# Kernel tuning notes

Hardware: AMD Instinct MI355X
Metric: run time of the kernel (lower is better)

Reference implementation:

```python
import jax, jax.numpy as jnp
import numpy as np

N_NODES = 1_000_000
N_EDGES = 16_000_000
N_GRAPHS = 256
IN_FEATS = 8
DIM = 1
N_LAYERS = 4


def setup_inputs() -> dict:
    key = jax.random.key(0)
    ks = jax.random.split(key, 16)
    x = jax.random.normal(ks[0], (N_NODES, IN_FEATS), dtype=jnp.float32)
    src = jax.random.randint(ks[1], (N_EDGES,), 0, N_NODES, dtype=jnp.int32)
    dst = jax.random.randint(ks[2], (N_EDGES,), 0, N_NODES, dtype=jnp.int32)
    graph_ids = jnp.sort(jax.random.randint(ks[3], (N_NODES,), 0, N_GRAPHS, dtype=jnp.int32))
    s = 1.0 / np.sqrt(IN_FEATS)
    # layer 0: in_feats -> 1 (neighbor GraphConv weight+bias, self linear no bias)
    W0n = jax.random.uniform(ks[4], (IN_FEATS, DIM), jnp.float32, -s, s)
    b0 = jnp.zeros((DIM,), jnp.float32)
    W0s = jax.random.uniform(ks[5], (IN_FEATS, DIM), jnp.float32, -s, s)
    # layers 1..3: 1 -> 1, stacked
    Wkn = jax.random.uniform(ks[6], (N_LAYERS - 1, DIM, DIM), jnp.float32, -1.0, 1.0)
    bk = jnp.zeros((N_LAYERS - 1, DIM), jnp.float32)
    Wks = jax.random.uniform(ks[7], (N_LAYERS - 1, DIM, DIM), jnp.float32, -1.0, 1.0)
    fc1_w = jax.random.uniform(ks[8], (DIM, 8), jnp.float32, -1.0, 1.0)
    fc1_b = jax.random.uniform(ks[9], (8,), jnp.float32, -1.0, 1.0)
    out_w = jax.random.uniform(ks[10], (8, 4), jnp.float32, -1.0 / np.sqrt(8), 1.0 / np.sqrt(8))
    out_b = jax.random.uniform(ks[11], (4,), jnp.float32, -1.0 / np.sqrt(8), 1.0 / np.sqrt(8))
    return {"x": x, "src": src, "dst": dst, "graph_ids": graph_ids, "num_graphs": N_GRAPHS,
            "W0n": W0n, "b0": b0, "W0s": W0s, "Wkn": Wkn, "bk": bk, "Wks": Wks,
            "fc1_w": fc1_w, "fc1_b": fc1_b, "out_w": out_w, "out_b": out_b}


def _graph_conv_wl(x, src, dst, Wn, bn, Ws, n_nodes):
    # GraphConvWL: sum-aggregated neighbor GraphConv (norm='none') + self linear.
    # Apply weight before aggregation (mathematically identical, and cheaper since out_dim=1).
    xw = x @ Wn                                            # [N, out]
    neigh = jax.ops.segment_sum(xw[src], dst, num_segments=n_nodes) + bn
    return neigh + x @ Ws


def reference(x, src, dst, graph_ids, num_graphs, W0n, b0, W0s, Wkn, bk, Wks, fc1_w, fc1_b, out_w, out_b):
    n = x.shape[0]
    h = jax.nn.relu(_graph_conv_wl(x, src, dst, W0n, b0, W0s, n))
    for i in range(Wkn.shape[0]):
        h = jax.nn.relu(_graph_conv_wl(h, src, dst, Wkn[i], bk[i], Wks[i], n))
    hg = jax.ops.segment_sum(h, graph_ids, num_segments=num_graphs)  # [G, 1] readout
    hg2 = jax.nn.sigmoid((hg @ fc1_w + fc1_b) * 1000.0)
    out = jax.nn.relu(hg2 @ out_w + out_b)
    return jax.nn.log_softmax(out, axis=1)
```

## Files before the change

### kernel.cpp

```cpp
#include <hip/hip_runtime.h>
#include <stdint.h>


static constexpr int NGRAPHS    = 256;
static constexpr int TB         = 256;
static constexpr int TB_P       = 512;
static constexpr int PGRID      = 256;
static constexpr int TB_A       = 1024;
static constexpr int BNODE_LOG  = 12;
static constexpr int BNODE      = 1 << BNODE_LOG;
static constexpr int MAXBUCK    = 256;
static constexpr int LOCAL_SHIFT = 20;


__global__ void node_init(const float4* __restrict__ x,
                          const float* __restrict__ W0n,
                          const float* __restrict__ W0s,
                          float* __restrict__ xw0,
                          float* __restrict__ s0,
                          int n_nodes) {
    int n = blockIdx.x * blockDim.x + threadIdx.x;
    if (n >= n_nodes) return;
    float4 a = x[2 * n];
    float4 b = x[2 * n + 1];
    float xn = a.x * W0n[0] + a.y * W0n[1] + a.z * W0n[2] + a.w * W0n[3] +
               b.x * W0n[4] + b.y * W0n[5] + b.z * W0n[6] + b.w * W0n[7];
    float xs = a.x * W0s[0] + a.y * W0s[1] + a.z * W0s[2] + a.w * W0s[3] +
               b.x * W0s[4] + b.y * W0s[5] + b.z * W0s[6] + b.w * W0s[7];
    xw0[n] = xn;
    s0[n] = xs;
}

__global__ void head(const float* __restrict__ hg,
                     const float* __restrict__ fc1_w,
                     const float* __restrict__ fc1_b,
                     const float* __restrict__ out_w,
                     const float* __restrict__ out_b,
                     float* __restrict__ out) {
    int gph = threadIdx.x;
    if (gph >= NGRAPHS) return;
    float hv = hg[gph];
    float o0 = out_b[0], o1 = out_b[1], o2 = out_b[2], o3 = out_b[3];
#pragma unroll
    for (int j = 0; j < 8; ++j) {
        float z = (hv * fc1_w[j] + fc1_b[j]) * 1000.0f;
        float sg = 1.0f / (1.0f + expf(-z));
        o0 += sg * out_w[j * 4 + 0];
        o1 += sg * out_w[j * 4 + 1];
        o2 += sg * out_w[j * 4 + 2];
        o3 += sg * out_w[j * 4 + 3];
    }
    o0 = fmaxf(o0, 0.0f); o1 = fmaxf(o1, 0.0f);
    o2 = fmaxf(o2, 0.0f); o3 = fmaxf(o3, 0.0f);
    float m = fmaxf(fmaxf(o0, o1), fmaxf(o2, o3));
    float s = expf(o0 - m) + expf(o1 - m) + expf(o2 - m) + expf(o3 - m);
    float l = logf(s);
    out[gph * 4 + 0] = o0 - m - l;
    out[gph * 4 + 1] = o1 - m - l;
    out[gph * 4 + 2] = o2 - m - l;
    out[gph * 4 + 3] = o3 - m - l;
}


__global__ void count_bins(const int* __restrict__ dst, int n_edges, int nbuck,
                           int* __restrict__ counts) {
    __shared__ int hist[MAXBUCK];
    for (int i = threadIdx.x; i < MAXBUCK; i += blockDim.x) hist[i] = 0;
    __syncthreads();
    const int4* dst4 = (const int4*)dst;
    int nquads = n_edges >> 2;
    int gtid = blockIdx.x * blockDim.x + threadIdx.x;
    int stride = gridDim.x * blockDim.x;
    for (int q = gtid; q < nquads; q += stride) {
        int4 d = dst4[q];
        atomicAdd(&hist[d.x >> BNODE_LOG], 1);
        atomicAdd(&hist[d.y >> BNODE_LOG], 1);
        atomicAdd(&hist[d.z >> BNODE_LOG], 1);
        atomicAdd(&hist[d.w >> BNODE_LOG], 1);
    }
    if (blockIdx.x == 0) {
        for (int e = (nquads << 2) + threadIdx.x; e < n_edges; e += blockDim.x)
            atomicAdd(&hist[dst[e] >> BNODE_LOG], 1);
    }
    __syncthreads();
    for (int i = threadIdx.x; i < nbuck; i += blockDim.x)
        if (hist[i]) atomicAdd(&counts[i], hist[i]);
}

__global__ void scan_offsets(const int* __restrict__ counts, int nbuck,
                             int* __restrict__ offs, int* __restrict__ cursor) {
    __shared__ int lds[MAXBUCK];
    int i = threadIdx.x;
    int c = (i < nbuck) ? counts[i] : 0;
    lds[i] = c;
    __syncthreads();
    for (int off = 1; off < MAXBUCK; off <<= 1) {
        int v = (i >= off) ? lds[i - off] : 0;
        __syncthreads();
        lds[i] += v;
        __syncthreads();
    }
    int excl = lds[i] - c;
    offs[i] = excl;
    if (i < nbuck) cursor[i] = excl;
    if (i == MAXBUCK - 1) offs[MAXBUCK] = lds[MAXBUCK - 1];
}

__global__ void place_edges(const int* __restrict__ src,
                            const int* __restrict__ dst,
                            int n_edges, int nbuck,
                            int* __restrict__ cursor,
                            uint32_t* __restrict__ sorted) {
    __shared__ int hist[MAXBUCK];
    for (int i = threadIdx.x; i < MAXBUCK; i += blockDim.x) hist[i] = 0;
    __syncthreads();

    const int nquads = n_edges >> 2;
    const int perq = (nquads + gridDim.x - 1) / gridDim.x;
    const int begq = blockIdx.x * perq;
    const int endq = min(begq + perq, nquads);
    const bool last = (blockIdx.x == gridDim.x - 1);
    const int tail_beg = nquads << 2;

    const int4* src4 = (const int4*)src;
    const int4* dst4 = (const int4*)dst;

    for (int q = begq + threadIdx.x; q < endq; q += blockDim.x) {
        int4 d = dst4[q];
        atomicAdd(&hist[d.x >> BNODE_LOG], 1);
        atomicAdd(&hist[d.y >> BNODE_LOG], 1);
        atomicAdd(&hist[d.z >> BNODE_LOG], 1);
        atomicAdd(&hist[d.w >> BNODE_LOG], 1);
    }
    if (last) {
        for (int e = tail_beg + threadIdx.x; e < n_edges; e += blockDim.x)
            atomicAdd(&hist[dst[e] >> BNODE_LOG], 1);
    }
    __syncthreads();
    for (int b = threadIdx.x; b < nbuck; b += blockDim.x) {
        int h = hist[b];
        hist[b] = h ? atomicAdd(&cursor[b], h) : 0;
    }
    __syncthreads();
    for (int q = begq + threadIdx.x; q < endq; q += blockDim.x) {
        int4 d = dst4[q];
        int4 s = src4[q];
        int p0 = atomicAdd(&hist[d.x >> BNODE_LOG], 1);
        int p1 = atomicAdd(&hist[d.y >> BNODE_LOG], 1);
        int p2 = atomicAdd(&hist[d.z >> BNODE_LOG], 1);
        int p3 = atomicAdd(&hist[d.w >> BNODE_LOG], 1);
        sorted[p0] = ((uint32_t)(d.x & (BNODE - 1)) << LOCAL_SHIFT) | (uint32_t)s.x;
        sorted[p1] = ((uint32_t)(d.y & (BNODE - 1)) << LOCAL_SHIFT) | (uint32_t)s.y;
        sorted[p2] = ((uint32_t)(d.z & (BNODE - 1)) << LOCAL_SHIFT) | (uint32_t)s.z;
        sorted[p3] = ((uint32_t)(d.w & (BNODE - 1)) << LOCAL_SHIFT) | (uint32_t)s.w;
    }
    if (last) {
        for (int e = tail_beg + threadIdx.x; e < n_edges; e += blockDim.x) {
            int d = dst[e];
            int pos = atomicAdd(&hist[d >> BNODE_LOG], 1);
            sorted[pos] = ((uint32_t)(d & (BNODE - 1)) << LOCAL_SHIFT) | (uint32_t)src[e];
        }
    }
}


__device__ __forceinline__ void bucket_accumulate(const uint32_t* __restrict__ sorted,
                                                  const int* __restrict__ offs,
                                                  const float* __restrict__ gsrc,
                                                  float* acc) {
    int b = blockIdx.x;
    for (int i = threadIdx.x; i < BNODE; i += TB_A) acc[i] = 0.0f;
    __syncthreads();
    int e = offs[b] + threadIdx.x;
    int eend = offs[b + 1];
    for (; e + 3 * TB_A < eend; e += 4 * TB_A) {
        uint32_t p0 = sorted[e];
        uint32_t p1 = sorted[e + TB_A];
        uint32_t p2 = sorted[e + 2 * TB_A];
        uint32_t p3 = sorted[e + 3 * TB_A];
        float v0 = gsrc[p0 & 0xFFFFFu];
        float v1 = gsrc[p1 & 0xFFFFFu];
        float v2 = gsrc[p2 & 0xFFFFFu];
        float v3 = gsrc[p3 & 0xFFFFFu];
        atomicAdd(&acc[p0 >> LOCAL_SHIFT], v0);
        atomicAdd(&acc[p1 >> LOCAL_SHIFT], v1);
        atomicAdd(&acc[p2 >> LOCAL_SHIFT], v2);
        atomicAdd(&acc[p3 >> LOCAL_SHIFT], v3);
    }
    for (; e < eend; e += TB_A) {
        uint32_t p = sorted[e];
        atomicAdd(&acc[p >> LOCAL_SHIFT], gsrc[p & 0xFFFFFu]);
    }
    __syncthreads();
}

__global__ void layer0_agg(const uint32_t* __restrict__ sorted,
                           const int* __restrict__ offs,
                           const float* __restrict__ xw0,
                           const float* __restrict__ s0,
                           const float* __restrict__ b0,
                           float* __restrict__ h_out,
                           int n_nodes) {
    __shared__ float acc[BNODE];
    bucket_accumulate(sorted, offs, xw0, acc);
    int base = blockIdx.x << BNODE_LOG;
    int nloc = min(BNODE, n_nodes - base);
    float bb = b0[0];
    for (int i = threadIdx.x; i < nloc; i += TB_A) {
        int n = base + i;
        h_out[n] = fmaxf(acc[i] + bb + s0[n], 0.0f);
    }
}

__global__ void layerk_agg(const uint32_t* __restrict__ sorted,
                           const int* __restrict__ offs,
                           const float* __restrict__ h_in,
                           const float* __restrict__ Wkn,
                           const float* __restrict__ bk,
                           const float* __restrict__ Wks,
                           int li,
                           float* __restrict__ h_out,
                           int n_nodes) {
    __shared__ float acc[BNODE];
    bucket_accumulate(sorted, offs, h_in, acc);
    int base = blockIdx.x << BNODE_LOG;
    int nloc = min(BNODE, n_nodes - base);
    float wn = Wkn[li], bb = bk[li], ws = Wks[li];
    for (int i = threadIdx.x; i < nloc; i += TB_A) {
        int n = base + i;
        h_out[n] = fmaxf(wn * acc[i] + bb + ws * h_in[n], 0.0f);
    }
}

__global__ void layer_last_readout(const uint32_t* __restrict__ sorted,
                                   const int* __restrict__ offs,
                                   const float* __restrict__ h_in,
                                   const int* __restrict__ graph_ids,
                                   const float* __restrict__ Wkn,
                                   const float* __restrict__ bk,
                                   const float* __restrict__ Wks,
                                   int li,
                                   float* __restrict__ hg,
                                   int n_nodes) {
    __shared__ float acc[BNODE];
    bucket_accumulate(sorted, offs, h_in, acc);
    int base = blockIdx.x << BNODE_LOG;
    int nloc = min(BNODE, n_nodes - base);
    float wn = Wkn[li], bb = bk[li], ws = Wks[li];
    for (int i = threadIdx.x; i < BNODE; i += TB_A) {
        float val = 0.0f;
        int g = -1;
        if (i < nloc) {
            int n = base + i;
            val = fmaxf(wn * acc[i] + bb + ws * h_in[n], 0.0f);
            g = graph_ids[n];
        }
        int g0 = __shfl(g, 0);
        unsigned long long same = __ballot(g == g0);
        if (same == ~0ULL) {
            for (int o = 32; o > 0; o >>= 1) val += __shfl_down(val, o);
            if ((threadIdx.x & 63) == 0 && g >= 0) atomicAdd(&hg[g], val);
        } else if (g >= 0) {
            atomicAdd(&hg[g], val);
        }
    }
}


__global__ void edge_scatter(const int4* __restrict__ src4,
                             const int4* __restrict__ dst4,
                             const float* __restrict__ val,
                             float* __restrict__ agg,
                             int nquads) {
    int t = blockIdx.x * blockDim.x + threadIdx.x;
    if (t >= nquads) return;
    int4 s = src4[t];
    int4 d = dst4[t];
    float v0 = val[s.x], v1 = val[s.y], v2 = val[s.z], v3 = val[s.w];
    atomicAdd(&agg[d.x], v0);
    atomicAdd(&agg[d.y], v1);
    atomicAdd(&agg[d.z], v2);
    atomicAdd(&agg[d.w], v3);
}

__global__ void node_l0(float* __restrict__ agg, const float* __restrict__ s0,
                        const float* __restrict__ b0, float* __restrict__ h, int n_nodes) {
    int n = blockIdx.x * blockDim.x + threadIdx.x;
    if (n >= n_nodes) return;
    h[n] = fmaxf(agg[n] + b0[0] + s0[n], 0.0f);
    agg[n] = 0.0f;
}

__global__ void node_lk(float* __restrict__ agg, float* __restrict__ h,
                        const float* __restrict__ Wkn, const float* __restrict__ bk,
                        const float* __restrict__ Wks, int li, int n_nodes) {
    int n = blockIdx.x * blockDim.x + threadIdx.x;
    if (n >= n_nodes) return;
    float v = Wkn[li] * agg[n] + bk[li] + Wks[li] * h[n];
    h[n] = fmaxf(v, 0.0f);
    agg[n] = 0.0f;
}

__global__ void node_l3_readout(const float* __restrict__ agg, const float* __restrict__ h,
                                const int* __restrict__ graph_ids,
                                const float* __restrict__ Wkn, const float* __restrict__ bk,
                                const float* __restrict__ Wks, float* __restrict__ hg,
                                int n_nodes) {
    int n = blockIdx.x * blockDim.x + threadIdx.x;
    float val = 0.0f;
    int g = -1;
    if (n < n_nodes) {
        val = fmaxf(Wkn[2] * agg[n] + bk[2] + Wks[2] * h[n], 0.0f);
        g = graph_ids[n];
    }
    int g0 = __shfl(g, 0);
    unsigned long long same = __ballot(g == g0);
    if (same == ~0ULL) {
        for (int o = 32; o > 0; o >>= 1) val += __shfl_down(val, o);
        if ((threadIdx.x & 63) == 0 && g >= 0) atomicAdd(&hg[g], val);
    } else if (g >= 0) {
        atomicAdd(&hg[g], val);
    }
}


extern "C" void kernel_launch(void* const* d_in, const int* in_sizes, int n_in,
                              void* d_out, int out_size, void* d_ws, size_t ws_size,
                              hipStream_t stream) {
    const float* x        = (const float*)d_in[0];
    const int*   src      = (const int*)d_in[1];
    const int*   dst      = (const int*)d_in[2];
    const int*   graphids = (const int*)d_in[3];
    const float* W0n   = (const float*)d_in[5];
    const float* b0    = (const float*)d_in[6];
    const float* W0s   = (const float*)d_in[7];
    const float* Wkn   = (const float*)d_in[8];
    const float* bk    = (const float*)d_in[9];
    const float* Wks   = (const float*)d_in[10];
    const float* fc1_w = (const float*)d_in[11];
    const float* fc1_b = (const float*)d_in[12];
    const float* out_w = (const float*)d_in[13];
    const float* out_b = (const float*)d_in[14];
    float* out = (float*)d_out;

    const int n_nodes = in_sizes[0] / 8;
    const int n_edges = in_sizes[1];
    const int nbuck   = (n_nodes + BNODE - 1) >> BNODE_LOG;
    const size_t NB   = (size_t)n_nodes * sizeof(float);

    const int node_blocks = (n_nodes + TB - 1) / TB;

    const size_t need = (size_t)n_edges * 4 + 4 * NB +
                        (MAXBUCK + (MAXBUCK + 1) + MAXBUCK + NGRAPHS) * sizeof(int) + 256;

    if (nbuck <= MAXBUCK && n_nodes <= (1 << 20) && ws_size >= need) {
        char* ws = (char*)d_ws;
        uint32_t* sorted = (uint32_t*)ws;                 ws += (size_t)n_edges * 4;
        float* xw0 = (float*)ws;                          ws += NB;
        float* s0  = (float*)ws;                          ws += NB;
        float* h_a = (float*)ws;                          ws += NB;
        float* h_b = (float*)ws;                          ws += NB;
        int* counts = (int*)ws;                           ws += MAXBUCK * sizeof(int);
        int* offs   = (int*)ws;                           ws += (MAXBUCK + 1) * sizeof(int);
        int* cursor = (int*)ws;                           ws += MAXBUCK * sizeof(int);
        float* hg   = (float*)ws;

        hipMemsetAsync(counts, 0, nbuck * sizeof(int), stream);
        hipMemsetAsync(hg, 0, NGRAPHS * sizeof(float), stream);

        node_init<<<node_blocks, TB, 0, stream>>>((const float4*)x, W0n, W0s, xw0, s0, n_nodes);
        count_bins<<<2048, TB, 0, stream>>>(dst, n_edges, nbuck, counts);
        scan_offsets<<<1, MAXBUCK, 0, stream>>>(counts, nbuck, offs, cursor);
        place_edges<<<PGRID, TB_P, 0, stream>>>(src, dst, n_edges, nbuck, cursor, sorted);

        layer0_agg<<<nbuck, TB_A, 0, stream>>>(sorted, offs, xw0, s0, b0, h_a, n_nodes);
        layerk_agg<<<nbuck, TB_A, 0, stream>>>(sorted, offs, h_a, Wkn, bk, Wks, 0, h_b, n_nodes);
        layerk_agg<<<nbuck, TB_A, 0, stream>>>(sorted, offs, h_b, Wkn, bk, Wks, 1, h_a, n_nodes);
        layer_last_readout<<<nbuck, TB_A, 0, stream>>>(sorted, offs, h_a, graphids, Wkn, bk, Wks, 2, hg, n_nodes);

        head<<<1, TB, 0, stream>>>(hg, fc1_w, fc1_b, out_w, out_b, out);
    } else {
        char* ws   = (char*)d_ws;
        float* agg = (float*)(ws);
        float* h   = (float*)(ws + NB);
        float* xw0 = (float*)(ws + 2 * NB);
        float* s0  = (float*)(ws + 3 * NB);
        float* hg  = (float*)(ws + 4 * NB);
        const int nquads = n_edges >> 2;
        const int edge_blocks = (nquads + TB - 1) / TB;

        hipMemsetAsync(agg, 0, NB, stream);
        hipMemsetAsync(hg, 0, NGRAPHS * sizeof(float), stream);

        node_init<<<node_blocks, TB, 0, stream>>>((const float4*)x, W0n, W0s, xw0, s0, n_nodes);
        edge_scatter<<<edge_blocks, TB, 0, stream>>>((const int4*)src, (const int4*)dst, xw0, agg, nquads);
        node_l0<<<node_blocks, TB, 0, stream>>>(agg, s0, b0, h, n_nodes);
        for (int li = 0; li < 2; ++li) {
            edge_scatter<<<edge_blocks, TB, 0, stream>>>((const int4*)src, (const int4*)dst, h, agg, nquads);
            node_lk<<<node_blocks, TB, 0, stream>>>(agg, h, Wkn, bk, Wks, li, n_nodes);
        }
        edge_scatter<<<edge_blocks, TB, 0, stream>>>((const int4*)src, (const int4*)dst, h, agg, nquads);
        node_l3_readout<<<node_blocks, TB, 0, stream>>>(agg, h, graphids, Wkn, bk, Wks, hg, n_nodes);
        head<<<1, TB, 0, stream>>>(hg, fc1_w, fc1_b, out_w, out_b, out);
    }
}
```

Measured before the change: 596.9 us.

## Split each bucket's edge aggregation across two blocks with separate reduce kernels

Each destination bucket's edge range is split in half and handled by two blocks, each writing a partial LDS accumulator to global memory. A separate reduce kernel per layer sums the two partials and applies the layer's epilogue. The goal is more blocks to fill the GPU, since 245 buckets is fewer than the CU count times occupancy. The inner loop is also unrolled to 8 loads, and place_edges gets twice as many blocks. The cost is four extra kernel launches plus a partial-buffer write and read per layer.

Result: slower. 638.0 us (+6.9%).

```diff
diff --git a/kernel.cpp b/kernel.cpp
--- a/kernel.cpp
+++ b/kernel.cpp
@@ -5,12 +5,13 @@
 static constexpr int NGRAPHS    = 256;
 static constexpr int TB         = 256;
 static constexpr int TB_P       = 512;
-static constexpr int PGRID      = 256;
+static constexpr int PGRID      = 512;
 static constexpr int TB_A       = 1024;
 static constexpr int BNODE_LOG  = 12;
 static constexpr int BNODE      = 1 << BNODE_LOG;
 static constexpr int MAXBUCK    = 256;
 static constexpr int LOCAL_SHIFT = 20;
+static constexpr int SPLIT      = 2;
 
 
 __global__ void node_init(const float4* __restrict__ x,
@@ -164,95 +165,113 @@
 }
 
 
-__device__ __forceinline__ void bucket_accumulate(const uint32_t* __restrict__ sorted,
-                                                  const int* __restrict__ offs,
-                                                  const float* __restrict__ gsrc,
-                                                  float* acc) {
-    int b = blockIdx.x;
+__global__ void agg_partial(const uint32_t* __restrict__ sorted,
+                            const int* __restrict__ offs,
+                            const float* __restrict__ gsrc,
+                            float* __restrict__ partial) {
+    __shared__ float acc[BNODE];
+    const int b = blockIdx.x;
+    const int k = b >> 1;
+    const int half = b & 1;
     for (int i = threadIdx.x; i < BNODE; i += TB_A) acc[i] = 0.0f;
     __syncthreads();
-    int e = offs[b] + threadIdx.x;
-    int eend = offs[b + 1];
-    for (; e + 3 * TB_A < eend; e += 4 * TB_A) {
+
+    const int off = offs[k];
+    const int len = offs[k + 1] - off;
+    const int hl  = (len + 1) >> 1;
+    const int beg = off + half * hl;
+    const int end = min(off + len, beg + hl);
+
+    int e = beg + threadIdx.x;
+    for (; e + 7 * TB_A < end; e += 8 * TB_A) {
         uint32_t p0 = sorted[e];
         uint32_t p1 = sorted[e + TB_A];
         uint32_t p2 = sorted[e + 2 * TB_A];
         uint32_t p3 = sorted[e + 3 * TB_A];
+        uint32_t p4 = sorted[e + 4 * TB_A];
+        uint32_t p5 = sorted[e + 5 * TB_A];
+        uint32_t p6 = sorted[e + 6 * TB_A];
+        uint32_t p7 = sorted[e + 7 * TB_A];
         float v0 = gsrc[p0 & 0xFFFFFu];
         float v1 = gsrc[p1 & 0xFFFFFu];
         float v2 = gsrc[p2 & 0xFFFFFu];
         float v3 = gsrc[p3 & 0xFFFFFu];
+        float v4 = gsrc[p4 & 0xFFFFFu];
+        float v5 = gsrc[p5 & 0xFFFFFu];
+        float v6 = gsrc[p6 & 0xFFFFFu];
+        float v7 = gsrc[p7 & 0xFFFFFu];
         atomicAdd(&acc[p0 >> LOCAL_SHIFT], v0);
         atomicAdd(&acc[p1 >> LOCAL_SHIFT], v1);
         atomicAdd(&acc[p2 >> LOCAL_SHIFT], v2);
         atomicAdd(&acc[p3 >> LOCAL_SHIFT], v3);
-    }
-    for (; e < eend; e += TB_A) {
+        atomicAdd(&acc[p4 >> LOCAL_SHIFT], v4);
+        atomicAdd(&acc[p5 >> LOCAL_SHIFT], v5);
+        atomicAdd(&acc[p6 >> LOCAL_SHIFT], v6);
+        atomicAdd(&acc[p7 >> LOCAL_SHIFT], v7);
+    }
+    for (; e < end; e += TB_A) {
         uint32_t p = sorted[e];
         atomicAdd(&acc[p >> LOCAL_SHIFT], gsrc[p & 0xFFFFFu]);
     }
     __syncthreads();
-}
-
-__global__ void layer0_agg(const uint32_t* __restrict__ sorted,
-                           const int* __restrict__ offs,
-                           const float* __restrict__ xw0,
-                           const float* __restrict__ s0,
-                           const float* __restrict__ b0,
-                           float* __restrict__ h_out,
-                           int n_nodes) {
-    __shared__ float acc[BNODE];
-    bucket_accumulate(sorted, offs, xw0, acc);
-    int base = blockIdx.x << BNODE_LOG;
+    float* o = partial + (size_t)b * BNODE;
+    for (int i = threadIdx.x; i < BNODE; i += TB_A) o[i] = acc[i];
+}
+
+__global__ void reduce_l0(const float* __restrict__ partial,
+                          const float* __restrict__ s0,
+                          const float* __restrict__ b0,
+                          float* __restrict__ h_out,
+                          int n_nodes) {
+    int k = blockIdx.x;
+    const float* pa = partial + (size_t)(2 * k) * BNODE;
+    const float* pb = pa + BNODE;
+    int base = k << BNODE_LOG;
     int nloc = min(BNODE, n_nodes - base);
     float bb = b0[0];
-    for (int i = threadIdx.x; i < nloc; i += TB_A) {
-        int n = base + i;
-        h_out[n] = fmaxf(acc[i] + bb + s0[n], 0.0f);
-    }
-}
-
-__global__ void layerk_agg(const uint32_t* __restrict__ sorted,
-                           const int* __restrict__ offs,
-                           const float* __restrict__ h_in,
-                           const float* __restrict__ Wkn,
-                           const float* __restrict__ bk,
-                           const float* __restrict__ Wks,
-                           int li,
-                           float* __restrict__ h_out,
-                           int n_nodes) {
-    __shared__ float acc[BNODE];
-    bucket_accumulate(sorted, offs, h_in, acc);
-    int base = blockIdx.x << BNODE_LOG;
+    for (int i = threadIdx.x; i < nloc; i += blockDim.x)
+        h_out[base + i] = fmaxf(pa[i] + pb[i] + bb + s0[base + i], 0.0f);
+}
+
+__global__ void reduce_lk(const float* __restrict__ partial,
+                          const float* __restrict__ h_in,
+                          const float* __restrict__ Wkn,
+                          const float* __restrict__ bk,
+                          const float* __restrict__ Wks,
+                          int li,
+                          float* __restrict__ h_out,
+                          int n_nodes) {
+    int k = blockIdx.x;
+    const float* pa = partial + (size_t)(2 * k) * BNODE;
+    const float* pb = pa + BNODE;
+    int base = k << BNODE_LOG;
     int nloc = min(BNODE, n_nodes - base);
     float wn = Wkn[li], bb = bk[li], ws = Wks[li];
-    for (int i = threadIdx.x; i < nloc; i += TB_A) {
-        int n = base + i;
-        h_out[n] = fmaxf(wn * acc[i] + bb + ws * h_in[n], 0.0f);
-    }
-}
-
-__global__ void layer_last_readout(const uint32_t* __restrict__ sorted,
-                                   const int* __restrict__ offs,
-                                   const float* __restrict__ h_in,
-                                   const int* __restrict__ graph_ids,
-                                   const float* __restrict__ Wkn,
-                                   const float* __restrict__ bk,
-                                   const float* __restrict__ Wks,
-                                   int li,
-                                   float* __restrict__ hg,
-                                   int n_nodes) {
-    __shared__ float acc[BNODE];
-    bucket_accumulate(sorted, offs, h_in, acc);
-    int base = blockIdx.x << BNODE_LOG;
+    for (int i = threadIdx.x; i < nloc; i += blockDim.x)
+        h_out[base + i] = fmaxf(wn * (pa[i] + pb[i]) + bb + ws * h_in[base + i], 0.0f);
+}
+
+__global__ void reduce_last(const float* __restrict__ partial,
+                            const float* __restrict__ h_in,
+                            const int* __restrict__ graph_ids,
+                            const float* __restrict__ Wkn,
+                            const float* __restrict__ bk,
+                            const float* __restrict__ Wks,
+                            int li,
+                            float* __restrict__ hg,
+                            int n_nodes) {
+    int k = blockIdx.x;
+    const float* pa = partial + (size_t)(2 * k) * BNODE;
+    const float* pb = pa + BNODE;
+    int base = k << BNODE_LOG;
     int nloc = min(BNODE, n_nodes - base);
     float wn = Wkn[li], bb = bk[li], ws = Wks[li];
-    for (int i = threadIdx.x; i < BNODE; i += TB_A) {
+    for (int i = threadIdx.x; i < BNODE; i += blockDim.x) {
         float val = 0.0f;
         int g = -1;
         if (i < nloc) {
             int n = base + i;
-            val = fmaxf(wn * acc[i] + bb + ws * h_in[n], 0.0f);
+            val = fmaxf(wn * (pa[i] + pb[i]) + bb + ws * h_in[n], 0.0f);
             g = graph_ids[n];
         }
         int g0 = __shfl(g, 0);
@@ -276,11 +295,10 @@
     if (t >= nquads) return;
     int4 s = src4[t];
     int4 d = dst4[t];
-    float v0 = val[s.x], v1 = val[s.y], v2 = val[s.z], v3 = val[s.w];
-    atomicAdd(&agg[d.x], v0);
-    atomicAdd(&agg[d.y], v1);
-    atomicAdd(&agg[d.z], v2);
-    atomicAdd(&agg[d.w], v3);
+    atomicAdd(&agg[d.x], val[s.x]);
+    atomicAdd(&agg[d.y], val[s.y]);
+    atomicAdd(&agg[d.z], val[s.z]);
+    atomicAdd(&agg[d.w], val[s.w]);
 }
 
 __global__ void node_l0(float* __restrict__ agg, const float* __restrict__ s0,
@@ -350,7 +368,8 @@
 
     const int node_blocks = (n_nodes + TB - 1) / TB;
 
-    const size_t need = (size_t)n_edges * 4 + 4 * NB +
+    const size_t partial_bytes = (size_t)SPLIT * MAXBUCK * BNODE * sizeof(float);
+    const size_t need = (size_t)n_edges * 4 + 4 * NB + partial_bytes +
                         (MAXBUCK + (MAXBUCK + 1) + MAXBUCK + NGRAPHS) * sizeof(int) + 256;
 
     if (nbuck <= MAXBUCK && n_nodes <= (1 << 20) && ws_size >= need) {
@@ -360,6 +379,7 @@
         float* s0  = (float*)ws;                          ws += NB;
         float* h_a = (float*)ws;                          ws += NB;
         float* h_b = (float*)ws;                          ws += NB;
+        float* partial = (float*)ws;                      ws += partial_bytes;
         int* counts = (int*)ws;                           ws += MAXBUCK * sizeof(int);
         int* offs   = (int*)ws;                           ws += (MAXBUCK + 1) * sizeof(int);
         int* cursor = (int*)ws;                           ws += MAXBUCK * sizeof(int);
@@ -373,10 +393,18 @@
         scan_offsets<<<1, MAXBUCK, 0, stream>>>(counts, nbuck, offs, cursor);
         place_edges<<<PGRID, TB_P, 0, stream>>>(src, dst, n_edges, nbuck, cursor, sorted);
 
-        layer0_agg<<<nbuck, TB_A, 0, stream>>>(sorted, offs, xw0, s0, b0, h_a, n_nodes);
-        layerk_agg<<<nbuck, TB_A, 0, stream>>>(sorted, offs, h_a, Wkn, bk, Wks, 0, h_b, n_nodes);
-        layerk_agg<<<nbuck, TB_A, 0, stream>>>(sorted, offs, h_b, Wkn, bk, Wks, 1, h_a, n_nodes);
-        layer_last_readout<<<nbuck, TB_A, 0, stream>>>(sorted, offs, h_a, graphids, Wkn, bk, Wks, 2, hg, n_nodes);
+        const int agrid = SPLIT * nbuck;
+        agg_partial<<<agrid, TB_A, 0, stream>>>(sorted, offs, xw0, partial);
+        reduce_l0<<<nbuck, TB_A, 0, stream>>>(partial, s0, b0, h_a, n_nodes);
+
+        agg_partial<<<agrid, TB_A, 0, stream>>>(sorted, offs, h_a, partial);
+        reduce_lk<<<nbuck, TB_A, 0, stream>>>(partial, h_a, Wkn, bk, Wks, 0, h_b, n_nodes);
+
+        agg_partial<<<agrid, TB_A, 0, stream>>>(sorted, offs, h_b, partial);
+        reduce_lk<<<nbuck, TB_A, 0, stream>>>(partial, h_b, Wkn, bk, Wks, 1, h_a, n_nodes);
+
+        agg_partial<<<agrid, TB_A, 0, stream>>>(sorted, offs, h_a, partial);
+        reduce_last<<<nbuck, TB_A, 0, stream>>>(partial, h_a, graphids, Wkn, bk, Wks, 2, hg, n_nodes);
 
         head<<<1, TB, 0, stream>>>(hg, fc1_w, fc1_b, out_w, out_b, out);
     } else {
```

## Replace two-pass bucket sort with per-chunk histograms and precomputed cursors

Applied to the files above, without the earlier changes.

The edge bucketing now records a per-chunk bucket histogram in a first kernel. A single-block scan turns those counts into bucket offsets plus a per-chunk starting cursor, so the placement kernel reads dst once and needs no global atomics and no second histogram pass over dst. The aggregation loop loads four packed edges at once as uint4 when aligned, and the aggregation kernels get launch bounds. Workspace buffers for the histograms overlap the node feature arrays, so node_init is moved after placement. The serial 256-iteration scan in one block adds a small latency.

Result: faster. 523.4 us, median of 2 (-12.3%).

```diff
diff --git a/kernel.cpp b/kernel.cpp
--- a/kernel.cpp
+++ b/kernel.cpp
@@ -2,14 +2,14 @@
 #include <stdint.h>
 
 
-static constexpr int NGRAPHS    = 256;
-static constexpr int TB         = 256;
-static constexpr int TB_P       = 512;
-static constexpr int PGRID      = 256;
-static constexpr int TB_A       = 1024;
-static constexpr int BNODE_LOG  = 12;
-static constexpr int BNODE      = 1 << BNODE_LOG;
-static constexpr int MAXBUCK    = 256;
+static constexpr int NGRAPHS   = 256;
+static constexpr int TB        = 256;
+static constexpr int TB_P      = 512;
+static constexpr int NCHUNK    = 256;
+static constexpr int TB_A      = 1024;
+static constexpr int BNODE_LOG = 12;
+static constexpr int BNODE     = 1 << BNODE_LOG;
+static constexpr int MAXBUCK   = 256;
 static constexpr int LOCAL_SHIFT = 20;
 
 
@@ -62,102 +62,92 @@
 }
 
 
-__global__ void count_bins(const int* __restrict__ dst, int n_edges, int nbuck,
-                           int* __restrict__ counts) {
+__global__ void count_chunks(const int* __restrict__ dst,
+                             int n_edges,
+                             int* __restrict__ chunk_hist) {
     __shared__ int hist[MAXBUCK];
     for (int i = threadIdx.x; i < MAXBUCK; i += blockDim.x) hist[i] = 0;
     __syncthreads();
-    const int4* dst4 = (const int4*)dst;
-    int nquads = n_edges >> 2;
-    int gtid = blockIdx.x * blockDim.x + threadIdx.x;
-    int stride = gridDim.x * blockDim.x;
-    for (int q = gtid; q < nquads; q += stride) {
-        int4 d = dst4[q];
+    const int nq = n_edges >> 2;
+    const int per = (nq + NCHUNK - 1) / NCHUNK;
+    const int b0 = blockIdx.x * per;
+    const int b1 = min(b0 + per, nq);
+    const bool last = (blockIdx.x == NCHUNK - 1);
+    const int4* d4 = (const int4*)dst;
+    for (int q = b0 + threadIdx.x; q < b1; q += blockDim.x) {
+        int4 d = d4[q];
         atomicAdd(&hist[d.x >> BNODE_LOG], 1);
         atomicAdd(&hist[d.y >> BNODE_LOG], 1);
         atomicAdd(&hist[d.z >> BNODE_LOG], 1);
         atomicAdd(&hist[d.w >> BNODE_LOG], 1);
     }
-    if (blockIdx.x == 0) {
-        for (int e = (nquads << 2) + threadIdx.x; e < n_edges; e += blockDim.x)
+    if (last) {
+        for (int e = (nq << 2) + threadIdx.x; e < n_edges; e += blockDim.x)
             atomicAdd(&hist[dst[e] >> BNODE_LOG], 1);
     }
     __syncthreads();
-    for (int i = threadIdx.x; i < nbuck; i += blockDim.x)
-        if (hist[i]) atomicAdd(&counts[i], hist[i]);
-}
-
-__global__ void scan_offsets(const int* __restrict__ counts, int nbuck,
-                             int* __restrict__ offs, int* __restrict__ cursor) {
+    for (int i = threadIdx.x; i < MAXBUCK; i += blockDim.x)
+        chunk_hist[blockIdx.x * MAXBUCK + i] = hist[i];
+}
+
+__global__ void chunk_scan(const int* __restrict__ chunk_hist, int nbuck,
+                           int* __restrict__ offs, int* __restrict__ cursors) {
     __shared__ int lds[MAXBUCK];
-    int i = threadIdx.x;
-    int c = (i < nbuck) ? counts[i] : 0;
-    lds[i] = c;
+    const int b = threadIdx.x;
+    int total = 0;
+    if (b < nbuck)
+        for (int c = 0; c < NCHUNK; ++c) total += chunk_hist[c * MAXBUCK + b];
+    lds[b] = total;
     __syncthreads();
     for (int off = 1; off < MAXBUCK; off <<= 1) {
-        int v = (i >= off) ? lds[i - off] : 0;
+        int v = (b >= off) ? lds[b - off] : 0;
         __syncthreads();
-        lds[i] += v;
+        lds[b] += v;
         __syncthreads();
     }
-    int excl = lds[i] - c;
-    offs[i] = excl;
-    if (i < nbuck) cursor[i] = excl;
-    if (i == MAXBUCK - 1) offs[MAXBUCK] = lds[MAXBUCK - 1];
-}
-
-__global__ void place_edges(const int* __restrict__ src,
-                            const int* __restrict__ dst,
-                            int n_edges, int nbuck,
-                            int* __restrict__ cursor,
-                            uint32_t* __restrict__ sorted) {
-    __shared__ int hist[MAXBUCK];
-    for (int i = threadIdx.x; i < MAXBUCK; i += blockDim.x) hist[i] = 0;
-    __syncthreads();
-
-    const int nquads = n_edges >> 2;
-    const int perq = (nquads + gridDim.x - 1) / gridDim.x;
-    const int begq = blockIdx.x * perq;
-    const int endq = min(begq + perq, nquads);
-    const bool last = (blockIdx.x == gridDim.x - 1);
-    const int tail_beg = nquads << 2;
-
-    const int4* src4 = (const int4*)src;
-    const int4* dst4 = (const int4*)dst;
-
-    for (int q = begq + threadIdx.x; q < endq; q += blockDim.x) {
-        int4 d = dst4[q];
-        atomicAdd(&hist[d.x >> BNODE_LOG], 1);
-        atomicAdd(&hist[d.y >> BNODE_LOG], 1);
-        atomicAdd(&hist[d.z >> BNODE_LOG], 1);
-        atomicAdd(&hist[d.w >> BNODE_LOG], 1);
-    }
-    if (last) {
-        for (int e = tail_beg + threadIdx.x; e < n_edges; e += blockDim.x)
-            atomicAdd(&hist[dst[e] >> BNODE_LOG], 1);
-    }
-    __syncthreads();
-    for (int b = threadIdx.x; b < nbuck; b += blockDim.x) {
-        int h = hist[b];
-        hist[b] = h ? atomicAdd(&cursor[b], h) : 0;
-    }
-    __syncthreads();
-    for (int q = begq + threadIdx.x; q < endq; q += blockDim.x) {
-        int4 d = dst4[q];
-        int4 s = src4[q];
-        int p0 = atomicAdd(&hist[d.x >> BNODE_LOG], 1);
-        int p1 = atomicAdd(&hist[d.y >> BNODE_LOG], 1);
-        int p2 = atomicAdd(&hist[d.z >> BNODE_LOG], 1);
-        int p3 = atomicAdd(&hist[d.w >> BNODE_LOG], 1);
+    int excl = lds[b] - total;
+    offs[b] = excl;
+    if (b == MAXBUCK - 1) offs[MAXBUCK] = lds[MAXBUCK - 1];
+    if (b < nbuck) {
+        int run = excl;
+        for (int c = 0; c < NCHUNK; ++c) {
+            cursors[c * MAXBUCK + b] = run;
+            run += chunk_hist[c * MAXBUCK + b];
+        }
+    }
+}
+
+__global__ void place1(const int* __restrict__ src,
+                       const int* __restrict__ dst,
+                       int n_edges,
+                       const int* __restrict__ cursors,
+                       uint32_t* __restrict__ sorted) {
+    __shared__ int cur[MAXBUCK];
+    for (int i = threadIdx.x; i < MAXBUCK; i += blockDim.x)
+        cur[i] = cursors[blockIdx.x * MAXBUCK + i];
+    __syncthreads();
+    const int nq = n_edges >> 2;
+    const int per = (nq + NCHUNK - 1) / NCHUNK;
+    const int b0 = blockIdx.x * per;
+    const int b1 = min(b0 + per, nq);
+    const bool last = (blockIdx.x == NCHUNK - 1);
+    const int4* s4 = (const int4*)src;
+    const int4* d4 = (const int4*)dst;
+    for (int q = b0 + threadIdx.x; q < b1; q += blockDim.x) {
+        int4 d = d4[q]; int4 s = s4[q];
+        int p0 = atomicAdd(&cur[d.x >> BNODE_LOG], 1);
+        int p1 = atomicAdd(&cur[d.y >> BNODE_LOG], 1);
+        int p2 = atomicAdd(&cur[d.z >> BNODE_LOG], 1);
+        int p3 = atomicAdd(&cur[d.w >> BNODE_LOG], 1);
         sorted[p0] = ((uint32_t)(d.x & (BNODE - 1)) << LOCAL_SHIFT) | (uint32_t)s.x;
         sorted[p1] = ((uint32_t)(d.y & (BNODE - 1)) << LOCAL_SHIFT) | (uint32_t)s.y;
         sorted[p2] = ((uint32_t)(d.z & (BNODE - 1)) << LOCAL_SHIFT) | (uint32_t)s.z;
         sorted[p3] = ((uint32_t)(d.w & (BNODE - 1)) << LOCAL_SHIFT) | (uint32_t)s.w;
     }
     if (last) {
-        for (int e = tail_beg + threadIdx.x; e < n_edges; e += blockDim.x) {
+        for (int e = (nq << 2) + threadIdx.x; e < n_edges; e += blockDim.x) {
             int d = dst[e];
-            int pos = atomicAdd(&hist[d >> BNODE_LOG], 1);
+            int pos = atomicAdd(&cur[d >> BNODE_LOG], 1);
             sorted[pos] = ((uint32_t)(d & (BNODE - 1)) << LOCAL_SHIFT) | (uint32_t)src[e];
         }
     }
@@ -165,44 +155,46 @@
 
 
 __device__ __forceinline__ void bucket_accumulate(const uint32_t* __restrict__ sorted,
-                                                  const int* __restrict__ offs,
+                                                  int beg, int end,
                                                   const float* __restrict__ gsrc,
                                                   float* acc) {
-    int b = blockIdx.x;
-    for (int i = threadIdx.x; i < BNODE; i += TB_A) acc[i] = 0.0f;
-    __syncthreads();
-    int e = offs[b] + threadIdx.x;
-    int eend = offs[b + 1];
-    for (; e + 3 * TB_A < eend; e += 4 * TB_A) {
-        uint32_t p0 = sorted[e];
-        uint32_t p1 = sorted[e + TB_A];
-        uint32_t p2 = sorted[e + 2 * TB_A];
-        uint32_t p3 = sorted[e + 3 * TB_A];
-        float v0 = gsrc[p0 & 0xFFFFFu];
-        float v1 = gsrc[p1 & 0xFFFFFu];
-        float v2 = gsrc[p2 & 0xFFFFFu];
-        float v3 = gsrc[p3 & 0xFFFFFu];
-        atomicAdd(&acc[p0 >> LOCAL_SHIFT], v0);
-        atomicAdd(&acc[p1 >> LOCAL_SHIFT], v1);
-        atomicAdd(&acc[p2 >> LOCAL_SHIFT], v2);
-        atomicAdd(&acc[p3 >> LOCAL_SHIFT], v3);
-    }
-    for (; e < eend; e += TB_A) {
-        uint32_t p = sorted[e];
-        atomicAdd(&acc[p >> LOCAL_SHIFT], gsrc[p & 0xFFFFFu]);
-    }
-    __syncthreads();
-}
-
-__global__ void layer0_agg(const uint32_t* __restrict__ sorted,
-                           const int* __restrict__ offs,
-                           const float* __restrict__ xw0,
-                           const float* __restrict__ s0,
-                           const float* __restrict__ b0,
-                           float* __restrict__ h_out,
-                           int n_nodes) {
+    const int tid = threadIdx.x;
+    for (int i = tid; i < BNODE; i += TB_A) acc[i] = 0.0f;
+    __syncthreads();
+    int vbeg = min((beg + 3) & ~3, end);
+    int vend = (vbeg < end) ? (end & ~3) : vbeg;
+    for (int e = beg + tid; e < vbeg; e += TB_A) {
+        uint32_t r = sorted[e];
+        atomicAdd(&acc[r >> LOCAL_SHIFT], gsrc[r & 0xFFFFFu]);
+    }
+    const uint4* sq = (const uint4*)sorted;
+    for (int q = (vbeg >> 2) + tid; q < (vend >> 2); q += TB_A) {
+        uint4 r = sq[q];
+        float v0 = gsrc[r.x & 0xFFFFFu];
+        float v1 = gsrc[r.y & 0xFFFFFu];
+        float v2 = gsrc[r.z & 0xFFFFFu];
+        float v3 = gsrc[r.w & 0xFFFFFu];
+        atomicAdd(&acc[r.x >> LOCAL_SHIFT], v0);
+        atomicAdd(&acc[r.y >> LOCAL_SHIFT], v1);
+        atomicAdd(&acc[r.z >> LOCAL_SHIFT], v2);
+        atomicAdd(&acc[r.w >> LOCAL_SHIFT], v3);
+    }
+    for (int e = max(vend, beg) + tid; e < end; e += TB_A) {
+        uint32_t r = sorted[e];
+        atomicAdd(&acc[r >> LOCAL_SHIFT], gsrc[r & 0xFFFFFu]);
+    }
+    __syncthreads();
+}
+
+__global__ __launch_bounds__(TB_A) void layer0_agg(const uint32_t* __restrict__ sorted,
+                                                   const int* __restrict__ offs,
+                                                   const float* __restrict__ xw0,
+                                                   const float* __restrict__ s0,
+                                                   const float* __restrict__ b0,
+                                                   float* __restrict__ h_out,
+                                                   int n_nodes) {
     __shared__ float acc[BNODE];
-    bucket_accumulate(sorted, offs, xw0, acc);
+    bucket_accumulate(sorted, offs[blockIdx.x], offs[blockIdx.x + 1], xw0, acc);
     int base = blockIdx.x << BNODE_LOG;
     int nloc = min(BNODE, n_nodes - base);
     float bb = b0[0];
@@ -212,17 +204,17 @@
     }
 }
 
-__global__ void layerk_agg(const uint32_t* __restrict__ sorted,
-                           const int* __restrict__ offs,
-                           const float* __restrict__ h_in,
-                           const float* __restrict__ Wkn,
-                           const float* __restrict__ bk,
-                           const float* __restrict__ Wks,
-                           int li,
-                           float* __restrict__ h_out,
-                           int n_nodes) {
+__global__ __launch_bounds__(TB_A) void layerk_agg(const uint32_t* __restrict__ sorted,
+                                                   const int* __restrict__ offs,
+                                                   const float* __restrict__ h_in,
+                                                   const float* __restrict__ Wkn,
+                                                   const float* __restrict__ bk,
+                                                   const float* __restrict__ Wks,
+                                                   int li,
+                                                   float* __restrict__ h_out,
+                                                   int n_nodes) {
     __shared__ float acc[BNODE];
-    bucket_accumulate(sorted, offs, h_in, acc);
+    bucket_accumulate(sorted, offs[blockIdx.x], offs[blockIdx.x + 1], h_in, acc);
     int base = blockIdx.x << BNODE_LOG;
     int nloc = min(BNODE, n_nodes - base);
     float wn = Wkn[li], bb = bk[li], ws = Wks[li];
@@ -232,18 +224,18 @@
     }
 }
 
-__global__ void layer_last_readout(const uint32_t* __restrict__ sorted,
-                                   const int* __restrict__ offs,
-                                   const float* __restrict__ h_in,
-                                   const int* __restrict__ graph_ids,
-                                   const float* __restrict__ Wkn,
-                                   const float* __restrict__ bk,
-                                   const float* __restrict__ Wks,
-                                   int li,
-                                   float* __restrict__ hg,
-                                   int n_nodes) {
+__global__ __launch_bounds__(TB_A) void layer_last_readout(const uint32_t* __restrict__ sorted,
+                                                           const int* __restrict__ offs,
+                                                           const float* __restrict__ h_in,
+                                                           const int* __restrict__ graph_ids,
+                                                           const float* __restrict__ Wkn,
+                                                           const float* __restrict__ bk,
+                                                           const float* __restrict__ Wks,
+                                                           int li,
+                                                           float* __restrict__ hg,
+                                                           int n_nodes) {
     __shared__ float acc[BNODE];
-    bucket_accumulate(sorted, offs, h_in, acc);
+    bucket_accumulate(sorted, offs[blockIdx.x], offs[blockIdx.x + 1], h_in, acc);
     int base = blockIdx.x << BNODE_LOG;
     int nloc = min(BNODE, n_nodes - base);
     float wn = Wkn[li], bb = bk[li], ws = Wks[li];
@@ -270,17 +262,14 @@
 __global__ void edge_scatter(const int4* __restrict__ src4,
                              const int4* __restrict__ dst4,
                              const float* __restrict__ val,
-                             float* __restrict__ agg,
-                             int nquads) {
+                             float* __restrict__ agg, int nquads) {
     int t = blockIdx.x * blockDim.x + threadIdx.x;
     if (t >= nquads) return;
-    int4 s = src4[t];
-    int4 d = dst4[t];
-    float v0 = val[s.x], v1 = val[s.y], v2 = val[s.z], v3 = val[s.w];
-    atomicAdd(&agg[d.x], v0);
-    atomicAdd(&agg[d.y], v1);
-    atomicAdd(&agg[d.z], v2);
-    atomicAdd(&agg[d.w], v3);
+    int4 s = src4[t]; int4 d = dst4[t];
+    atomicAdd(&agg[d.x], val[s.x]);
+    atomicAdd(&agg[d.y], val[s.y]);
+    atomicAdd(&agg[d.z], val[s.z]);
+    atomicAdd(&agg[d.w], val[s.w]);
 }
 
 __global__ void node_l0(float* __restrict__ agg, const float* __restrict__ s0,
@@ -346,32 +335,37 @@
     const int n_nodes = in_sizes[0] / 8;
     const int n_edges = in_sizes[1];
     const int nbuck   = (n_nodes + BNODE - 1) >> BNODE_LOG;
-    const size_t NB   = (size_t)n_nodes * sizeof(float);
-
     const int node_blocks = (n_nodes + TB - 1) / TB;
 
-    const size_t need = (size_t)n_edges * 4 + 4 * NB +
-                        (MAXBUCK + (MAXBUCK + 1) + MAXBUCK + NGRAPHS) * sizeof(int) + 256;
-
-    if (nbuck <= MAXBUCK && n_nodes <= (1 << 20) && ws_size >= need) {
+    const size_t E4   = (size_t)n_edges * 4;
+    const size_t NBP  = (size_t)(1 << 20) * sizeof(float);
+    const size_t hist_bytes = (size_t)2 * NCHUNK * MAXBUCK * sizeof(int);
+    const size_t ov_bytes = 4 * NBP;
+    const size_t tail_bytes = (MAXBUCK + 1) * sizeof(int) + NGRAPHS * sizeof(float) + 256;
+    const size_t need_full = E4 + ov_bytes + tail_bytes;
+
+    const bool shape_ok = (nbuck <= MAXBUCK) && (n_nodes <= (1 << 20)) &&
+                          (n_edges >= 4) && (ov_bytes >= hist_bytes);
+
+    if (shape_ok && ws_size >= need_full) {
         char* ws = (char*)d_ws;
-        uint32_t* sorted = (uint32_t*)ws;                 ws += (size_t)n_edges * 4;
-        float* xw0 = (float*)ws;                          ws += NB;
-        float* s0  = (float*)ws;                          ws += NB;
-        float* h_a = (float*)ws;                          ws += NB;
-        float* h_b = (float*)ws;                          ws += NB;
-        int* counts = (int*)ws;                           ws += MAXBUCK * sizeof(int);
-        int* offs   = (int*)ws;                           ws += (MAXBUCK + 1) * sizeof(int);
-        int* cursor = (int*)ws;                           ws += MAXBUCK * sizeof(int);
-        float* hg   = (float*)ws;
-
-        hipMemsetAsync(counts, 0, nbuck * sizeof(int), stream);
+        uint32_t* sorted = (uint32_t*)ws;                  ws += E4;
+        char* ov = ws;                                     ws += ov_bytes;
+        float* xw0 = (float*)(ov);
+        float* s0  = (float*)(ov + NBP);
+        float* h_a = (float*)(ov + 2 * NBP);
+        float* h_b = (float*)(ov + 3 * NBP);
+        int* offs  = (int*)ws;                             ws += (MAXBUCK + 1) * sizeof(int);
+        float* hg  = (float*)ws;
+        int* chunk_hist = (int*)ov;
+        int* cursors    = chunk_hist + NCHUNK * MAXBUCK;
+
         hipMemsetAsync(hg, 0, NGRAPHS * sizeof(float), stream);
 
+        count_chunks<<<NCHUNK, TB_P, 0, stream>>>(dst, n_edges, chunk_hist);
+        chunk_scan<<<1, MAXBUCK, 0, stream>>>(chunk_hist, nbuck, offs, cursors);
+        place1<<<NCHUNK, TB_P, 0, stream>>>(src, dst, n_edges, cursors, sorted);
         node_init<<<node_blocks, TB, 0, stream>>>((const float4*)x, W0n, W0s, xw0, s0, n_nodes);
-        count_bins<<<2048, TB, 0, stream>>>(dst, n_edges, nbuck, counts);
-        scan_offsets<<<1, MAXBUCK, 0, stream>>>(counts, nbuck, offs, cursor);
-        place_edges<<<PGRID, TB_P, 0, stream>>>(src, dst, n_edges, nbuck, cursor, sorted);
 
         layer0_agg<<<nbuck, TB_A, 0, stream>>>(sorted, offs, xw0, s0, b0, h_a, n_nodes);
         layerk_agg<<<nbuck, TB_A, 0, stream>>>(sorted, offs, h_a, Wkn, bk, Wks, 0, h_b, n_nodes);
@@ -380,6 +374,7 @@
 
         head<<<1, TB, 0, stream>>>(hg, fc1_w, fc1_b, out_w, out_b, out);
     } else {
+        const size_t NB = (size_t)n_nodes * sizeof(float);
         char* ws   = (char*)d_ws;
         float* agg = (float*)(ws);
         float* h   = (float*)(ws + NB);
```
